# Optimization experiments

Hardware: AMD Instinct MI355X
Metric: run time of the kernel (lower is better)

Reference implementation:

```python
import jax, jax.numpy as jnp
from jax import lax
import numpy as np

B, P, N = 4, 12000, 100   # batch, max_pillars, max_points_per_pillar
H, W = 108, 124           # pseudo-image size from forward()
DN = ('NCHW', 'HWIO', 'NCHW')


def _conv(x, k, b):
    y = lax.conv_general_dilated(x, k, (1, 1), 'SAME', dimension_numbers=DN)
    return y + b[None, :, None, None]


def _cbr(x, k, b, s, t):
    # Conv2d + folded BatchNorm2d (eval: per-channel scale/shift) + ReLU
    y = _conv(x, k, b)
    return jax.nn.relu(y * s[None, :, None, None] + t[None, :, None, None])


def _pool(x):
    return lax.reduce_window(x, -jnp.inf, lax.max, (1, 1, 2, 2), (1, 1, 2, 2), 'VALID')


def setup_inputs() -> dict:
    key = jax.random.key(0)
    ks = iter(jax.random.split(key, 64))
    d = {}
    d['pillars'] = jax.random.normal(next(ks), (B, P, N, 9), jnp.float32)

    def w(shape, scale=0.05):
        return jax.random.normal(next(ks), shape, jnp.float32) * scale

    d['w1'] = w((9, 64)); d['b1'] = w((64,))
    d['s1'] = 1.0 + w((64,)); d['t1'] = w((64,))
    d['w2'] = w((64, 64)); d['b2'] = w((64,))
    d['s2'] = 1.0 + w((64,)); d['t2'] = w((64,))
    chans = [(64, 64), (64, 64), (64, 128), (128, 128), (128, 256), (256, 256)]
    for i, (ci, co) in enumerate(chans, 1):
        d['ck%d' % i] = w((3, 3, ci, co)); d['cb%d' % i] = w((co,))
        d['cs%d' % i] = 1.0 + w((co,)); d['ct%d' % i] = w((co,))
    d['hk1'] = w((3, 3, 256, 256)); d['hb1'] = w((256,))
    d['hk2'] = w((1, 1, 256, 10)); d['hb2'] = w((10,))
    d['num_points'] = jax.random.randint(next(ks), (B, P), 0, 100, jnp.int32)
    return d


def reference(pillars, w1, b1, s1, t1, w2, b2, s2, t2,
              ck1, cb1, cs1, ct1, ck2, cb2, cs2, ct2,
              ck3, cb3, cs3, ct3, ck4, cb4, cs4, ct4,
              ck5, cb5, cs5, ct5, ck6, cb6, cs6, ct6,
              hk1, hb1, hk2, hb2, num_points):
    # pillar feature net: Linear+BN(folded)+ReLU x2, batched over all points  [B,P,N,9] -> [B,P,N,64]
    h = jax.nn.relu((pillars @ w1 + b1) * s1 + t1)
    h = jax.nn.relu((h @ w2 + b2) * s2 + t2)
    # masked segment-max over the variable-length point groups
    mask = jnp.arange(N)[None, None, :] < num_points[:, :, None]          # [B,P,N]
    neg = jnp.finfo(h.dtype).min
    feat = jnp.max(jnp.where(mask[..., None], h, neg), axis=2)            # [B,P,64]
    valid = num_points > 0
    feat = jnp.where(valid[..., None], feat, 0.0)
    cnt = jnp.maximum(jnp.sum(valid, axis=1), 1).astype(feat.dtype)       # [B]
    mean = jnp.sum(feat, axis=1) / cnt[:, None]                           # [B,64]
    # nearest-interpolate a 1x1 map to HxW == broadcast
    x = jnp.broadcast_to(mean[:, :, None, None], (pillars.shape[0], 64, H, W))
    # 2D backbone
    x = _cbr(x, ck1, cb1, cs1, ct1); x = _cbr(x, ck2, cb2, cs2, ct2); x = _pool(x)
    x = _cbr(x, ck3, cb3, cs3, ct3); x = _cbr(x, ck4, cb4, cs4, ct4); x = _pool(x)
    x = _cbr(x, ck5, cb5, cs5, ct5); x = _cbr(x, ck6, cb6, cs6, ct6)
    # detection head
    y = jax.nn.relu(_conv(x, hk1, hb1))
    return _conv(y, hk2, hb2)   # [B, num_classes+7=10, 27, 31]
```

## Files before the change

kernel.cpp:

```cpp
#include <hip/hip_runtime.h>

typedef __bf16 vbf8 __attribute__((ext_vector_type(8)));
typedef unsigned short us8 __attribute__((ext_vector_type(8)));
typedef float f32x4 __attribute__((ext_vector_type(4)));
typedef float f32x4u __attribute__((ext_vector_type(4), aligned(4)));

#define NBLK 64

__device__ __forceinline__ int caseof(int h, int H, int e) {
  if (h < 0 || h >= H) return -1;
  if (h < e) return h;
  if (h >= H - e) return h - (H - 1) + 2 * e;
  return e;
}
__device__ __forceinline__ int repof(int i, int H, int eo) {
  return (i <= eo) ? i : H - 1 - 2 * eo + i;
}

__device__ __forceinline__ vbf8 max8(vbf8 a, vbf8 b) {
  us8 ua = __builtin_bit_cast(us8, a), ub = __builtin_bit_cast(us8, b);
  us8 o;
#pragma unroll
  for (int e = 0; e < 8; ++e) o[e] = ua[e] > ub[e] ? ua[e] : ub[e];
  return __builtin_bit_cast(vbf8, o);
}

__device__ __forceinline__ void gridbar(int* bar) {
  __syncthreads();
  if (threadIdx.x == 0) {
    int* cnt = bar; int* gen = bar + 1;
    int g = __hip_atomic_fetch_add(gen, 0, __ATOMIC_RELAXED, __HIP_MEMORY_SCOPE_AGENT);
    if (__hip_atomic_fetch_add(cnt, 1, __ATOMIC_ACQ_REL, __HIP_MEMORY_SCOPE_AGENT) == NBLK - 1) {
      __hip_atomic_fetch_add(cnt, -NBLK, __ATOMIC_RELAXED, __HIP_MEMORY_SCOPE_AGENT);
      __hip_atomic_fetch_add(gen, 1, __ATOMIC_RELEASE, __HIP_MEMORY_SCOPE_AGENT);
    } else {
      while (__hip_atomic_fetch_add(gen, 0, __ATOMIC_RELAXED, __HIP_MEMORY_SCOPE_AGENT) == g)
        __builtin_amdgcn_s_sleep(32);
    }
  }
  __syncthreads();
  __builtin_amdgcn_fence(__ATOMIC_ACQUIRE, "agent");
}

__global__ void setup_kernel(const float* __restrict__ w1, const float* __restrict__ b1,
                             const float* __restrict__ s1, const float* __restrict__ t1,
                             const float* __restrict__ w2, const float* __restrict__ b2,
                             const float* __restrict__ s2, const float* __restrict__ t2,
                             __bf16* __restrict__ wfrag, float* __restrict__ be2f) {
  int l = threadIdx.x;
  int s = l & 15, g = l >> 4;
#pragma unroll
  for (int m = 0; m < 4; ++m) {
    int c = 32 * (m & 1) + 8 * (s >> 2) + 4 * (m >> 1) + (s & 3);
#pragma unroll
    for (int e = 0; e < 8; ++e) {
      int k = g * 8 + e;
      float v = 0.f;
      if (k < 9)       v = w1[k * 64 + c] * s1[c];
      else if (k == 9) v = fmaf(b1[c], s1[c], t1[c]);
      wfrag[(m * 64 + l) * 8 + e] = (__bf16)v;
    }
    int co = s + 16 * m;
#pragma unroll
    for (int e = 0; e < 8; ++e) {
      int k = g * 8 + e;
      wfrag[((4 + m) * 64 + l) * 8 + e] = (__bf16)(w2[k * 64 + co] * s2[co]);
      wfrag[((8 + m) * 64 + l) * 8 + e] = (__bf16)(w2[(32 + k) * 64 + co] * s2[co]);
    }
    be2f[m * 64 + l] = fmaf(b2[co], s2[co], t2[co]);
  }
}

__global__ __launch_bounds__(256) void convw_kernel(
    const float* __restrict__ k1, const float* __restrict__ k2,
    const float* __restrict__ k3, const float* __restrict__ k4,
    const float* __restrict__ k5, const float* __restrict__ k6,
    const float* __restrict__ kh, __bf16* __restrict__ wT) {
  __shared__ float tile[64][65];
  const int tCI[7]    = {64, 64, 64, 128, 128, 256, 256};
  const int tCO[7]    = {64, 64, 128, 128, 256, 256, 256};
  const int tOFF[7]   = {0, 36864, 73728, 147456, 294912, 589824, 1179648};
  const int tTILES[7] = {9, 9, 18, 36, 72, 144, 144};
  int bid = blockIdx.x;
  int ti = 0, acc = 0;
  while (ti < 6 && bid >= acc + tTILES[ti]) { acc += tTILES[ti]; ++ti; }
  int lt = bid - acc;
  int CI = tCI[ti], CO = tCO[ti];
  const float* src;
  if (ti == 0) src = k1; else if (ti == 1) src = k2; else if (ti == 2) src = k3;
  else if (ti == 3) src = k4; else if (ti == 4) src = k5; else if (ti == 5) src = k6;
  else src = kh;
  int cot = CO / 64, tpt = (CI / 64) * cot;
  int tap = lt / tpt; int r2 = lt - tap * tpt;
  int ci0 = (r2 / cot) * 64, co0 = (r2 % cot) * 64;
  const float* sp = src + (size_t)(tap * CI + ci0) * CO + co0;
  int t = threadIdx.x;
  int lr = t >> 6, lc = t & 63;
#pragma unroll
  for (int rr = 0; rr < 64; rr += 4)
    tile[rr + lr][lc] = sp[(size_t)(rr + lr) * CO + lc];
  __syncthreads();
  __bf16* dst = wT + tOFF[ti] + ((size_t)tap * CO + co0) * CI + ci0;
#pragma unroll
  for (int rr = 0; rr < 64; rr += 4)
    dst[(size_t)(rr + lr) * CI + lc] = (__bf16)tile[lc][rr + lr];
}

__global__ __launch_bounds__(256) void pillar_kernel(
    const float* __restrict__ pil, const int* __restrict__ npt,
    const __bf16* __restrict__ wfrag, const float* __restrict__ be2f,
    float* __restrict__ partial, int* __restrict__ pcnt)
{
  __shared__ float redf[4][64];
  __shared__ int redc[4];
  const int tid = threadIdx.x;
  const int wv = tid >> 6, lane = tid & 63;
  const int s = lane & 15, g = lane >> 4;
  const int wid = blockIdx.x * 4 + wv;
  const int b = wid / 6000;
  const int p0 = (wid - b * 6000) * 2;

  vbf8 w1f[4], w2f0[4], w2f1[4];
  float be2[4];
#pragma unroll
  for (int m = 0; m < 4; ++m) {
    w1f[m]  = *(const vbf8*)(wfrag + ((0 + m) * 64 + lane) * 8);
    w2f0[m] = *(const vbf8*)(wfrag + ((4 + m) * 64 + lane) * 8);
    w2f1[m] = *(const vbf8*)(wfrag + ((8 + m) * 64 + lane) * 8);
    be2[m] = be2f[m * 64 + lane];
  }

  float fsum[4] = {0.f, 0.f, 0.f, 0.f};
  int cnt = 0;

  for (int i = 0; i < 2; ++i) {
    int pidx = b * 12000 + p0 + i;
    int np = npt[pidx];
    if (np <= 0) continue;
    ++cnt;
    float feat[4][4];
#pragma unroll
    for (int n = 0; n < 4; ++n)
#pragma unroll
      for (int r = 0; r < 4; ++r) feat[n][r] = 0.f;

    int ngrp = (np + 15) >> 4;
    const float* pbase = pil + (size_t)pidx * 900;
    const float* pp0 = pbase + s * 9;
    f32x4u lo = *(const f32x4u*)pp0;
    f32x4u hi = *(const f32x4u*)(pp0 + 4);
    float v8 = pp0[8];
    for (int grp = 0; grp < ngrp; ++grp) {
      int g2 = min(grp + 1, ngrp - 1);
      int ptn = min(g2 * 16 + s, 99);
      const float* ppn = pbase + ptn * 9;
      f32x4u nlo = *(const f32x4u*)ppn;
      f32x4u nhi = *(const f32x4u*)(ppn + 4);
      float nv8 = ppn[8];

      vbf8 b1f;
      b1f[0] = (__bf16)(g == 0 ? lo[0] : (g == 1 ? v8 : 0.f));
      b1f[1] = (__bf16)(g == 0 ? lo[1] : (g == 1 ? 1.0f : 0.f));
      b1f[2] = (__bf16)(g == 0 ? lo[2] : 0.f);
      b1f[3] = (__bf16)(g == 0 ? lo[3] : 0.f);
      b1f[4] = (__bf16)(g == 0 ? hi[0] : 0.f);
      b1f[5] = (__bf16)(g == 0 ? hi[1] : 0.f);
      b1f[6] = (__bf16)(g == 0 ? hi[2] : 0.f);
      b1f[7] = (__bf16)(g == 0 ? hi[3] : 0.f);

      const f32x4 z = {0.f, 0.f, 0.f, 0.f};
      f32x4 d1[4];
#pragma unroll
      for (int m = 0; m < 4; ++m)
        d1[m] = __builtin_amdgcn_mfma_f32_16x16x32_bf16(w1f[m], b1f, z, 0, 0, 0);

      vbf8 a2f0, a2f1;
#pragma unroll
      for (int r = 0; r < 4; ++r) {
        a2f0[r]     = (__bf16)fmaxf(d1[0][r], 0.f);
        a2f1[r]     = (__bf16)fmaxf(d1[1][r], 0.f);
        a2f0[4 + r] = (__bf16)fmaxf(d1[2][r], 0.f);
        a2f1[4 + r] = (__bf16)fmaxf(d1[3][r], 0.f);
      }

      f32x4 d2[4];
#pragma unroll
      for (int n = 0; n < 4; ++n) {
        f32x4 cb = {be2[n], be2[n], be2[n], be2[n]};
        d2[n] = __builtin_amdgcn_mfma_f32_16x16x32_bf16(a2f0, w2f0[n], cb, 0, 0, 0);
        d2[n] = __builtin_amdgcn_mfma_f32_16x16x32_bf16(a2f1, w2f1[n], d2[n], 0, 0, 0);
      }
      if (((grp + 1) << 4) <= np) {
#pragma unroll
        for (int n = 0; n < 4; ++n)
#pragma unroll
          for (int r = 0; r < 4; ++r) feat[n][r] = fmaxf(feat[n][r], d2[n][r]);
      } else {
#pragma unroll
        for (int n = 0; n < 4; ++n)
#pragma unroll
          for (int r = 0; r < 4; ++r) {
            float vv = (grp * 16 + 4 * g + r < np) ? d2[n][r] : 0.f;
            feat[n][r] = fmaxf(feat[n][r], vv);
          }
      }
      lo = nlo; hi = nhi; v8 = nv8;
    }
#pragma unroll
    for (int n = 0; n < 4; ++n) {
      float m = fmaxf(fmaxf(feat[n][0], feat[n][1]), fmaxf(feat[n][2], feat[n][3]));
      m = fmaxf(m, __shfl_xor(m, 16));
      m = fmaxf(m, __shfl_xor(m, 32));
      fsum[n] += m;
    }
  }
  if (g == 0) {
#pragma unroll
    for (int n = 0; n < 4; ++n) redf[wv][s + 16 * n] = fsum[n];
  }
  if (lane == 0) redc[wv] = cnt;
  __syncthreads();
  if (tid < 64) {
    float tot = redf[0][tid] + redf[1][tid] + redf[2][tid] + redf[3][tid];
    partial[blockIdx.x * 64 + tid] = tot;
    if (tid == 0) pcnt[blockIdx.x] = redc[0] + redc[1] + redc[2] + redc[3];
  }
}

__global__ void mean_kernel(const float* __restrict__ partial,
                            const int* __restrict__ pcnt,
                            __bf16* __restrict__ x0,
                            __bf16* __restrict__ zbuf, int* __restrict__ bar) {
  int b = blockIdx.x, t = threadIdx.x;
  if (b == 0) {
    zbuf[t] = (__bf16)0.f;
    if (t < 2) bar[t] = 0;
  }
  int c = t & 63, q = t >> 6;
  float sum = 0.f;
  for (int w = q; w < 1500; w += 4) sum += partial[(b * 1500 + w) * 64 + c];
  int cl = 0;
  for (int w = t; w < 1500; w += 256) cl += pcnt[b * 1500 + w];
  __shared__ float sh[256];
  __shared__ int shc[256];
  sh[t] = sum; shc[t] = cl;
  __syncthreads();
  for (int o = 128; o > 0; o >>= 1) {
    if (t < o) shc[t] += shc[t + o];
    __syncthreads();
  }
  if (t < 64) {
    float tot = sh[t] + sh[t + 64] + sh[t + 128] + sh[t + 192];
    x0[b * 64 + t] = (__bf16)(tot / (float)(shc[0] > 0 ? shc[0] : 1));
  }
}

template <int CI, int CO, int H, int EIN, bool POOL, bool HAS_BN, bool OUT_F32>
__device__ __forceinline__ void caseconv_dev(
    int wid, const __bf16* __restrict__ xin, const __bf16* __restrict__ wt,
    const float* __restrict__ cb, const float* __restrict__ cs,
    const float* __restrict__ ct, __bf16* __restrict__ yout,
    float* __restrict__ yf32, const __bf16* __restrict__ zbuf)
{
  constexpr int EV   = POOL ? (EIN + 1) / 2 : EIN;
  constexpr int EOUT = EV + 1;
  constexpr int NBI  = 2 * EIN + 1;
  constexpr int HX   = POOL ? 2 * H : H;
  constexpr int NBO  = 2 * EOUT + 1;
  constexpr int M    = NBO * NBO * 4;
  constexpr int NT   = CO / 16;
  constexpr int KC   = CI / 32;
  constexpr int MT   = (M + 31) / 32;
  if (wid >= MT * NT) return;
  const int lane = threadIdx.x & 63;
  const int s = lane & 15, g = lane >> 4;
  const int nt = wid % NT, mt = wid / NT;

  int reph[2], repw[2], bsel[2];
#pragma unroll
  for (int mf = 0; mf < 2; ++mf) {
    int m = mt * 32 + mf * 16 + s; if (m >= M) m = M - 1;
    bsel[mf] = m & 3; int q = m >> 2;
    int bw = q % NBO, bh = q / NBO;
    reph[mf] = repof(bh, H, EOUT); repw[mf] = repof(bw, H, EOUT);
  }

  f32x4 acc0 = {0.f, 0.f, 0.f, 0.f}, acc1 = {0.f, 0.f, 0.f, 0.f};
#pragma unroll
  for (int tap = 0; tap < 9; ++tap) {
    const int dh = tap / 3, dw = tap % 3;
    const __bf16* wtap = wt + ((size_t)tap * CO + nt * 16) * CI + 8 * g;
    const __bf16* base[2][POOL ? 4 : 1];
#pragma unroll
    for (int mf = 0; mf < 2; ++mf) {
      int vh = reph[mf] + dh - 1, vw = repw[mf] + dw - 1;
      if constexpr (POOL) {
        bool valid = (vh >= 0) && (vh < H) && (vw >= 0) && (vw < H);
        int h0 = 0, h1 = 0, w0 = 0, w1 = 0;
        if (valid) {
          h0 = caseof(2 * vh, HX, EIN); h1 = caseof(2 * vh + 1, HX, EIN);
          w0 = caseof(2 * vw, HX, EIN); w1 = caseof(2 * vw + 1, HX, EIN);
        }
        base[mf][0] = valid ? xin + (size_t)((h0 * NBI + w0) * 4 + bsel[mf]) * CI : zbuf;
        base[mf][1] = valid ? xin + (size_t)((h0 * NBI + w1) * 4 + bsel[mf]) * CI : zbuf;
        base[mf][2] = valid ? xin + (size_t)((h1 * NBI + w0) * 4 + bsel[mf]) * CI : zbuf;
        base[mf][3] = valid ? xin + (size_t)((h1 * NBI + w1) * 4 + bsel[mf]) * CI : zbuf;
      } else {
        int jh = caseof(vh, H, EIN), jw = caseof(vw, H, EIN);
        bool v = (jh >= 0) && (jw >= 0);
        base[mf][0] = v ? xin + (size_t)((jh * NBI + jw) * 4 + bsel[mf]) * CI : zbuf;
      }
    }
#pragma unroll
    for (int ck = 0; ck < KC; ++ck) {
      vbf8 a0, a1;
      if constexpr (POOL) {
        a0 = max8(max8(*(const vbf8*)(base[0][0] + ck * 32 + 8 * g),
                       *(const vbf8*)(base[0][1] + ck * 32 + 8 * g)),
                  max8(*(const vbf8*)(base[0][2] + ck * 32 + 8 * g),
                       *(const vbf8*)(base[0][3] + ck * 32 + 8 * g)));
        a1 = max8(max8(*(const vbf8*)(base[1][0] + ck * 32 + 8 * g),
                       *(const vbf8*)(base[1][1] + ck * 32 + 8 * g)),
                  max8(*(const vbf8*)(base[1][2] + ck * 32 + 8 * g),
                       *(const vbf8*)(base[1][3] + ck * 32 + 8 * g)));
      } else {
        a0 = *(const vbf8*)(base[0][0] + ck * 32 + 8 * g);
        a1 = *(const vbf8*)(base[1][0] + ck * 32 + 8 * g);
      }
      vbf8 bb = *(const vbf8*)(wtap + (size_t)s * CI + ck * 32);
      acc0 = __builtin_amdgcn_mfma_f32_16x16x32_bf16(a0, bb, acc0, 0, 0, 0);
      acc1 = __builtin_amdgcn_mfma_f32_16x16x32_bf16(a1, bb, acc1, 0, 0, 0);
    }
  }

  int co = nt * 16 + s;
  float sc, sh;
  if (HAS_BN) { sc = cs[co]; sh = fmaf(cb[co], sc, ct[co]); }
  else        { sc = 1.f;    sh = cb[co]; }
#pragma unroll
  for (int mf = 0; mf < 2; ++mf) {
    f32x4 acc = mf ? acc1 : acc0;
#pragma unroll
    for (int r = 0; r < 4; ++r) {
      int m = mt * 32 + mf * 16 + 4 * g + r;
      if (m < M) {
        float v = fmaxf(fmaf(acc[r], sc, sh), 0.f);
        if constexpr (OUT_F32) yf32[(size_t)m * CO + co] = v;
        else                   yout[(size_t)m * CO + co] = (__bf16)v;
      }
    }
  }
}

__device__ __forceinline__ void headscatter_dev(int gtid, const float* __restrict__ x,
                                                const float* __restrict__ wk,
                                                const float* __restrict__ bias,
                                                float* __restrict__ out) {
  for (int idx = gtid; idx < 4 * 10 * 27 * 31; idx += NBLK * 256) {
    int c = idx % 31;
    int r = (idx / 31) % 27;
    int ch = (idx / (31 * 27)) % 10;
    int b = idx / (31 * 27 * 10);
    int rr = (r <= 7) ? r : ((r >= 20) ? r - 11 : 7);
    int cc = (c <= 7) ? c : ((c >= 24) ? c - 15 : 7);
    int ph = caseof(rr, 16, 5), pw = caseof(cc, 16, 5);
    const float* xr = x + (size_t)((ph * 11 + pw) * 4 + b) * 256;
    float a0 = 0.f, a1 = 0.f, a2 = 0.f, a3 = 0.f;
#pragma unroll 4
    for (int ci = 0; ci < 256; ci += 4) {
      float4 in4 = *(const float4*)(xr + ci);
      a0 = fmaf(in4.x, wk[(ci + 0) * 10 + ch], a0);
      a1 = fmaf(in4.y, wk[(ci + 1) * 10 + ch], a1);
      a2 = fmaf(in4.z, wk[(ci + 2) * 10 + ch], a2);
      a3 = fmaf(in4.w, wk[(ci + 3) * 10 + ch], a3);
    }
    out[idx] = (a0 + a1) + (a2 + a3) + bias[ch];
  }
}

__global__ __launch_bounds__(256) void backbone_kernel(
    const __bf16* __restrict__ X0, __bf16* __restrict__ X1, __bf16* __restrict__ X2,
    __bf16* __restrict__ X3, __bf16* __restrict__ X4, __bf16* __restrict__ X5,
    __bf16* __restrict__ X6, float* __restrict__ XH,
    const __bf16* wt1, const __bf16* wt2, const __bf16* wt3, const __bf16* wt4,
    const __bf16* wt5, const __bf16* wt6, const __bf16* wth,
    const float* cb1, const float* cs1, const float* ct1,
    const float* cb2, const float* cs2, const float* ct2,
    const float* cb3, const float* cs3, const float* ct3,
    const float* cb4, const float* cs4, const float* ct4,
    const float* cb5, const float* cs5, const float* ct5,
    const float* cb6, const float* cs6, const float* ct6,
    const float* hb1, const float* hk2, const float* hb2,
    const __bf16* __restrict__ zbuf, int* __restrict__ bar, float* __restrict__ out)
{
  const int wid = blockIdx.x * 4 + (threadIdx.x >> 6);
  const int gtid = blockIdx.x * 256 + threadIdx.x;

  caseconv_dev<64, 64, 64, 0, false, true, false>(wid, X0, wt1, cb1, cs1, ct1, X1, nullptr, zbuf);
  gridbar(bar);
  caseconv_dev<64, 64, 64, 1, false, true, false>(wid, X1, wt2, cb2, cs2, ct2, X2, nullptr, zbuf);
  gridbar(bar);
  caseconv_dev<64, 128, 32, 2, true, true, false>(wid, X2, wt3, cb3, cs3, ct3, X3, nullptr, zbuf);
  gridbar(bar);
  caseconv_dev<128, 128, 32, 2, false, true, false>(wid, X3, wt4, cb4, cs4, ct4, X4, nullptr, zbuf);
  gridbar(bar);
  caseconv_dev<128, 256, 16, 3, true, true, false>(wid, X4, wt5, cb5, cs5, ct5, X5, nullptr, zbuf);
  gridbar(bar);
  caseconv_dev<256, 256, 16, 3, false, true, false>(wid, X5, wt6, cb6, cs6, ct6, X6, nullptr, zbuf);
  gridbar(bar);
  caseconv_dev<256, 256, 16, 4, false, false, true>(wid, X6, wth, hb1, nullptr, nullptr, nullptr, XH, zbuf);
  gridbar(bar);
  headscatter_dev(gtid, XH, hk2, hb2, out);
}

extern "C" void kernel_launch(void* const* d_in, const int* in_sizes, int n_in,
                              void* d_out, int out_size, void* d_ws, size_t ws_size,
                              hipStream_t stream) {
  (void)in_sizes; (void)n_in; (void)out_size; (void)ws_size;
  const float* pillars = (const float*)d_in[0];
  const float* w1 = (const float*)d_in[1];
  const float* b1 = (const float*)d_in[2];
  const float* s1 = (const float*)d_in[3];
  const float* t1 = (const float*)d_in[4];
  const float* w2 = (const float*)d_in[5];
  const float* b2 = (const float*)d_in[6];
  const float* s2 = (const float*)d_in[7];
  const float* t2 = (const float*)d_in[8];
  const float* ck[6], *cbv[6], *csv[6], *ctv[6];
  for (int i = 0; i < 6; ++i) {
    ck[i]  = (const float*)d_in[9 + i * 4];
    cbv[i] = (const float*)d_in[10 + i * 4];
    csv[i] = (const float*)d_in[11 + i * 4];
    ctv[i] = (const float*)d_in[12 + i * 4];
  }
  const float* hk1 = (const float*)d_in[33];
  const float* hb1 = (const float*)d_in[34];
  const float* hk2 = (const float*)d_in[35];
  const float* hb2 = (const float*)d_in[36];
  const int* num_points = (const int*)d_in[37];
  float* out = (float*)d_out;

  char* wsb = (char*)d_ws;
  size_t off = 0;
  auto alloc = [&](size_t n) { char* p = wsb + off; off = (off + n + 255) & ~(size_t)255; return p; };
  float*  ppart = (float*)alloc(1536000);
  int*    pcnt  = (int*)alloc(24000);
  __bf16* wfrag = (__bf16*)alloc(12288);
  float*  be2f  = (float*)alloc(1024);
  __bf16* wT    = (__bf16*)alloc(3538944);
  __bf16* zbuf  = (__bf16*)alloc(512);
  int*    bar   = (int*)alloc(256);
  __bf16* X0    = (__bf16*)alloc(512);
  __bf16* X1    = (__bf16*)alloc(4608);
  __bf16* X2    = (__bf16*)alloc(12800);
  __bf16* X3    = (__bf16*)alloc(25600);
  __bf16* X4    = (__bf16*)alloc(50176);
  __bf16* X5    = (__bf16*)alloc(100352);
  __bf16* X6    = (__bf16*)alloc(165888);
  float*  XH    = (float*)alloc(495616);

  __bf16* wt1 = wT + 0;       __bf16* wt2 = wT + 36864;
  __bf16* wt3 = wT + 73728;   __bf16* wt4 = wT + 147456;
  __bf16* wt5 = wT + 294912;  __bf16* wt6 = wT + 589824;
  __bf16* wth = wT + 1179648;

  setup_kernel<<<1, 64, 0, stream>>>(w1, b1, s1, t1, w2, b2, s2, t2, wfrag, be2f);
  convw_kernel<<<432, 256, 0, stream>>>(ck[0], ck[1], ck[2], ck[3], ck[4], ck[5],
                                        hk1, wT);
  pillar_kernel<<<6000, 256, 0, stream>>>(pillars, num_points, wfrag, be2f,
                                          ppart, pcnt);
  mean_kernel<<<4, 256, 0, stream>>>(ppart, pcnt, X0, zbuf, bar);
  backbone_kernel<<<NBLK, 256, 0, stream>>>(
      X0, X1, X2, X3, X4, X5, X6, XH,
      wt1, wt2, wt3, wt4, wt5, wt6, wth,
      cbv[0], csv[0], ctv[0], cbv[1], csv[1], ctv[1],
      cbv[2], csv[2], ctv[2], cbv[3], csv[3], ctv[3],
      cbv[4], csv[4], ctv[4], cbv[5], csv[5], ctv[5],
      hb1, hk2, hb2, zbuf, bar, out);
}
```

Baseline: 390.5 us.

## Merge setup kernels, fuse mean and conv1-conv2 into backbone via LDS

Folds setup_kernel into the weight-transpose kernel as an extra block, removes mean_kernel by computing the per-batch mean inside the persistent backbone kernel, and fuses conv1 and conv2 per batch through shared memory to drop a grid barrier. It also halves the persistent grid to 32 blocks with a strided work loop and reworks the grid barrier to use plain loads/stores with shorter sleeps. This targets launch overhead and barrier latency in a latency-bound tail. The cost is less parallelism for the larger convs, and with fewer blocks each wave loops over more tiles.

```diff
diff --git a/kernel.cpp b/kernel.cpp
--- a/kernel.cpp
+++ b/kernel.cpp
@@ -5,7 +5,7 @@
 typedef float f32x4 __attribute__((ext_vector_type(4)));
 typedef float f32x4u __attribute__((ext_vector_type(4), aligned(4)));
 
-#define NBLK 64
+#define NBLK 32
 
 __device__ __forceinline__ int caseof(int h, int H, int e) {
   if (h < 0 || h >= H) return -1;
@@ -29,54 +29,64 @@
   __syncthreads();
   if (threadIdx.x == 0) {
     int* cnt = bar; int* gen = bar + 1;
-    int g = __hip_atomic_fetch_add(gen, 0, __ATOMIC_RELAXED, __HIP_MEMORY_SCOPE_AGENT);
+    int g = __hip_atomic_load(gen, __ATOMIC_RELAXED, __HIP_MEMORY_SCOPE_SYSTEM);
     if (__hip_atomic_fetch_add(cnt, 1, __ATOMIC_ACQ_REL, __HIP_MEMORY_SCOPE_AGENT) == NBLK - 1) {
-      __hip_atomic_fetch_add(cnt, -NBLK, __ATOMIC_RELAXED, __HIP_MEMORY_SCOPE_AGENT);
-      __hip_atomic_fetch_add(gen, 1, __ATOMIC_RELEASE, __HIP_MEMORY_SCOPE_AGENT);
+      __hip_atomic_store(cnt, 0, __ATOMIC_RELAXED, __HIP_MEMORY_SCOPE_AGENT);
+      __hip_atomic_store(gen, g + 1, __ATOMIC_RELEASE, __HIP_MEMORY_SCOPE_SYSTEM);
     } else {
-      while (__hip_atomic_fetch_add(gen, 0, __ATOMIC_RELAXED, __HIP_MEMORY_SCOPE_AGENT) == g)
-        __builtin_amdgcn_s_sleep(32);
+      while (__hip_atomic_load(gen, __ATOMIC_RELAXED, __HIP_MEMORY_SCOPE_SYSTEM) == g)
+        __builtin_amdgcn_s_sleep(4);
+      __builtin_amdgcn_fence(__ATOMIC_ACQUIRE, "agent");
     }
   }
   __syncthreads();
-  __builtin_amdgcn_fence(__ATOMIC_ACQUIRE, "agent");
-}
-
-__global__ void setup_kernel(const float* __restrict__ w1, const float* __restrict__ b1,
-                             const float* __restrict__ s1, const float* __restrict__ t1,
-                             const float* __restrict__ w2, const float* __restrict__ b2,
-                             const float* __restrict__ s2, const float* __restrict__ t2,
-                             __bf16* __restrict__ wfrag, float* __restrict__ be2f) {
-  int l = threadIdx.x;
-  int s = l & 15, g = l >> 4;
-#pragma unroll
-  for (int m = 0; m < 4; ++m) {
-    int c = 32 * (m & 1) + 8 * (s >> 2) + 4 * (m >> 1) + (s & 3);
-#pragma unroll
-    for (int e = 0; e < 8; ++e) {
-      int k = g * 8 + e;
-      float v = 0.f;
-      if (k < 9)       v = w1[k * 64 + c] * s1[c];
-      else if (k == 9) v = fmaf(b1[c], s1[c], t1[c]);
-      wfrag[(m * 64 + l) * 8 + e] = (__bf16)v;
-    }
-    int co = s + 16 * m;
-#pragma unroll
-    for (int e = 0; e < 8; ++e) {
-      int k = g * 8 + e;
-      wfrag[((4 + m) * 64 + l) * 8 + e] = (__bf16)(w2[k * 64 + co] * s2[co]);
-      wfrag[((8 + m) * 64 + l) * 8 + e] = (__bf16)(w2[(32 + k) * 64 + co] * s2[co]);
-    }
-    be2f[m * 64 + l] = fmaf(b2[co], s2[co], t2[co]);
-  }
-}
-
-__global__ __launch_bounds__(256) void convw_kernel(
+}
+
+__global__ __launch_bounds__(256) void prep_kernel(
     const float* __restrict__ k1, const float* __restrict__ k2,
     const float* __restrict__ k3, const float* __restrict__ k4,
     const float* __restrict__ k5, const float* __restrict__ k6,
-    const float* __restrict__ kh, __bf16* __restrict__ wT) {
+    const float* __restrict__ kh, __bf16* __restrict__ wT,
+    const float* __restrict__ w1, const float* __restrict__ b1,
+    const float* __restrict__ s1, const float* __restrict__ t1,
+    const float* __restrict__ w2, const float* __restrict__ b2,
+    const float* __restrict__ s2, const float* __restrict__ t2,
+    __bf16* __restrict__ wfrag, float* __restrict__ be2f,
+    __bf16* __restrict__ zbuf, int* __restrict__ bar) {
   __shared__ float tile[64][65];
+  if (blockIdx.x == 432) {
+    int l = threadIdx.x;
+    if (l < 64) {
+      int s = l & 15, g = l >> 4;
+#pragma unroll
+      for (int m = 0; m < 4; ++m) {
+        int c = 32 * (m & 1) + 8 * (s >> 2) + 4 * (m >> 1) + (s & 3);
+#pragma unroll
+        for (int e = 0; e < 8; ++e) {
+          int k = g * 8 + e;
+          float v = 0.f;
+          if (k < 9)       v = w1[k * 64 + c] * s1[c];
+          else if (k == 9) v = fmaf(b1[c], s1[c], t1[c]);
+          wfrag[(m * 64 + l) * 8 + e] = (__bf16)v;
+        }
+        int co = s + 16 * m;
+#pragma unroll
+        for (int e = 0; e < 8; ++e) {
+          int k = g * 8 + e;
+          wfrag[((4 + m) * 64 + l) * 8 + e] = (__bf16)(w2[k * 64 + co] * s2[co]);
+          wfrag[((8 + m) * 64 + l) * 8 + e] = (__bf16)(w2[(32 + k) * 64 + co] * s2[co]);
+        }
+        be2f[m * 64 + l] = fmaf(b2[co], s2[co], t2[co]);
+      }
+    } else if (l >= 64 && l < 128) {
+      int z = l - 64;
+#pragma unroll
+      for (int i = 0; i < 4; ++i) zbuf[z * 4 + i] = (__bf16)0.f;
+    } else if (l == 128) {
+      bar[0] = 0; bar[1] = 0;
+    }
+    return;
+  }
   const int tCI[7]    = {64, 64, 64, 128, 128, 256, 256};
   const int tCO[7]    = {64, 64, 128, 128, 256, 256, 256};
   const int tOFF[7]   = {0, 36864, 73728, 147456, 294912, 589824, 1179648};
@@ -227,37 +237,9 @@
   }
 }
 
-__global__ void mean_kernel(const float* __restrict__ partial,
-                            const int* __restrict__ pcnt,
-                            __bf16* __restrict__ x0,
-                            __bf16* __restrict__ zbuf, int* __restrict__ bar) {
-  int b = blockIdx.x, t = threadIdx.x;
-  if (b == 0) {
-    zbuf[t] = (__bf16)0.f;
-    if (t < 2) bar[t] = 0;
-  }
-  int c = t & 63, q = t >> 6;
-  float sum = 0.f;
-  for (int w = q; w < 1500; w += 4) sum += partial[(b * 1500 + w) * 64 + c];
-  int cl = 0;
-  for (int w = t; w < 1500; w += 256) cl += pcnt[b * 1500 + w];
-  __shared__ float sh[256];
-  __shared__ int shc[256];
-  sh[t] = sum; shc[t] = cl;
-  __syncthreads();
-  for (int o = 128; o > 0; o >>= 1) {
-    if (t < o) shc[t] += shc[t + o];
-    __syncthreads();
-  }
-  if (t < 64) {
-    float tot = sh[t] + sh[t + 64] + sh[t + 128] + sh[t + 192];
-    x0[b * 64 + t] = (__bf16)(tot / (float)(shc[0] > 0 ? shc[0] : 1));
-  }
-}
-
 template <int CI, int CO, int H, int EIN, bool POOL, bool HAS_BN, bool OUT_F32>
 __device__ __forceinline__ void caseconv_dev(
-    int wid, const __bf16* __restrict__ xin, const __bf16* __restrict__ wt,
+    int wid0, const __bf16* __restrict__ xin, const __bf16* __restrict__ wt,
     const float* __restrict__ cb, const float* __restrict__ cs,
     const float* __restrict__ ct, __bf16* __restrict__ yout,
     float* __restrict__ yf32, const __bf16* __restrict__ zbuf)
@@ -271,117 +253,93 @@
   constexpr int NT   = CO / 16;
   constexpr int KC   = CI / 32;
   constexpr int MT   = (M + 31) / 32;
-  if (wid >= MT * NT) return;
   const int lane = threadIdx.x & 63;
   const int s = lane & 15, g = lane >> 4;
-  const int nt = wid % NT, mt = wid / NT;
-
-  int reph[2], repw[2], bsel[2];
-#pragma unroll
-  for (int mf = 0; mf < 2; ++mf) {
-    int m = mt * 32 + mf * 16 + s; if (m >= M) m = M - 1;
-    bsel[mf] = m & 3; int q = m >> 2;
-    int bw = q % NBO, bh = q / NBO;
-    reph[mf] = repof(bh, H, EOUT); repw[mf] = repof(bw, H, EOUT);
-  }
-
-  f32x4 acc0 = {0.f, 0.f, 0.f, 0.f}, acc1 = {0.f, 0.f, 0.f, 0.f};
-#pragma unroll
-  for (int tap = 0; tap < 9; ++tap) {
-    const int dh = tap / 3, dw = tap % 3;
-    const __bf16* wtap = wt + ((size_t)tap * CO + nt * 16) * CI + 8 * g;
-    const __bf16* base[2][POOL ? 4 : 1];
+
+  for (int wid = wid0; wid < MT * NT; wid += NBLK * 4) {
+    const int nt = wid % NT, mt = wid / NT;
+    int reph[2], repw[2], bsel[2];
 #pragma unroll
     for (int mf = 0; mf < 2; ++mf) {
-      int vh = reph[mf] + dh - 1, vw = repw[mf] + dw - 1;
-      if constexpr (POOL) {
-        bool valid = (vh >= 0) && (vh < H) && (vw >= 0) && (vw < H);
-        int h0 = 0, h1 = 0, w0 = 0, w1 = 0;
-        if (valid) {
-          h0 = caseof(2 * vh, HX, EIN); h1 = caseof(2 * vh + 1, HX, EIN);
-          w0 = caseof(2 * vw, HX, EIN); w1 = caseof(2 * vw + 1, HX, EIN);
-        }
-        base[mf][0] = valid ? xin + (size_t)((h0 * NBI + w0) * 4 + bsel[mf]) * CI : zbuf;
-        base[mf][1] = valid ? xin + (size_t)((h0 * NBI + w1) * 4 + bsel[mf]) * CI : zbuf;
-        base[mf][2] = valid ? xin + (size_t)((h1 * NBI + w0) * 4 + bsel[mf]) * CI : zbuf;
-        base[mf][3] = valid ? xin + (size_t)((h1 * NBI + w1) * 4 + bsel[mf]) * CI : zbuf;
-      } else {
-        int jh = caseof(vh, H, EIN), jw = caseof(vw, H, EIN);
-        bool v = (jh >= 0) && (jw >= 0);
-        base[mf][0] = v ? xin + (size_t)((jh * NBI + jw) * 4 + bsel[mf]) * CI : zbuf;
-      }
-    }
-#pragma unroll
-    for (int ck = 0; ck < KC; ++ck) {
-      vbf8 a0, a1;
-      if constexpr (POOL) {
-        a0 = max8(max8(*(const vbf8*)(base[0][0] + ck * 32 + 8 * g),
-                       *(const vbf8*)(base[0][1] + ck * 32 + 8 * g)),
-                  max8(*(const vbf8*)(base[0][2] + ck * 32 + 8 * g),
-                       *(const vbf8*)(base[0][3] + ck * 32 + 8 * g)));
-        a1 = max8(max8(*(const vbf8*)(base[1][0] + ck * 32 + 8 * g),
-                       *(const vbf8*)(base[1][1] + ck * 32 + 8 * g)),
-                  max8(*(const vbf8*)(base[1][2] + ck * 32 + 8 * g),
-                       *(const vbf8*)(base[1][3] + ck * 32 + 8 * g)));
-      } else {
-        a0 = *(const vbf8*)(base[0][0] + ck * 32 + 8 * g);
-        a1 = *(const vbf8*)(base[1][0] + ck * 32 + 8 * g);
-      }
-      vbf8 bb = *(const vbf8*)(wtap + (size_t)s * CI + ck * 32);
-      acc0 = __builtin_amdgcn_mfma_f32_16x16x32_bf16(a0, bb, acc0, 0, 0, 0);
-      acc1 = __builtin_amdgcn_mfma_f32_16x16x32_bf16(a1, bb, acc1, 0, 0, 0);
-    }
-  }
-
-  int co = nt * 16 + s;
-  float sc, sh;
-  if (HAS_BN) { sc = cs[co]; sh = fmaf(cb[co], sc, ct[co]); }
-  else        { sc = 1.f;    sh = cb[co]; }
-#pragma unroll
-  for (int mf = 0; mf < 2; ++mf) {
-    f32x4 acc = mf ? acc1 : acc0;
-#pragma unroll
-    for (int r = 0; r < 4; ++r) {
-      int m = mt * 32 + mf * 16 + 4 * g + r;
-      if (m < M) {
-        float v = fmaxf(fmaf(acc[r], sc, sh), 0.f);
-        if constexpr (OUT_F32) yf32[(size_t)m * CO + co] = v;
-        else                   yout[(size_t)m * CO + co] = (__bf16)v;
-      }
-    }
-  }
-}
-
-__device__ __forceinline__ void headscatter_dev(int gtid, const float* __restrict__ x,
-                                                const float* __restrict__ wk,
-                                                const float* __restrict__ bias,
-                                                float* __restrict__ out) {
-  for (int idx = gtid; idx < 4 * 10 * 27 * 31; idx += NBLK * 256) {
-    int c = idx % 31;
-    int r = (idx / 31) % 27;
-    int ch = (idx / (31 * 27)) % 10;
-    int b = idx / (31 * 27 * 10);
-    int rr = (r <= 7) ? r : ((r >= 20) ? r - 11 : 7);
-    int cc = (c <= 7) ? c : ((c >= 24) ? c - 15 : 7);
-    int ph = caseof(rr, 16, 5), pw = caseof(cc, 16, 5);
-    const float* xr = x + (size_t)((ph * 11 + pw) * 4 + b) * 256;
-    float a0 = 0.f, a1 = 0.f, a2 = 0.f, a3 = 0.f;
-#pragma unroll 4
-    for (int ci = 0; ci < 256; ci += 4) {
-      float4 in4 = *(const float4*)(xr + ci);
-      a0 = fmaf(in4.x, wk[(ci + 0) * 10 + ch], a0);
-      a1 = fmaf(in4.y, wk[(ci + 1) * 10 + ch], a1);
-      a2 = fmaf(in4.z, wk[(ci + 2) * 10 + ch], a2);
-      a3 = fmaf(in4.w, wk[(ci + 3) * 10 + ch], a3);
-    }
-    out[idx] = (a0 + a1) + (a2 + a3) + bias[ch];
+      int m = mt * 32 + mf * 16 + s; if (m >= M) m = M - 1;
+      bsel[mf] = m & 3; int q = m >> 2;
+      int bw = q % NBO, bh = q / NBO;
+      reph[mf] = repof(bh, H, EOUT); repw[mf] = repof(bw, H, EOUT);
+    }
+
+    f32x4 acc0 = {0.f, 0.f, 0.f, 0.f}, acc1 = {0.f, 0.f, 0.f, 0.f};
+#pragma unroll
+    for (int tap = 0; tap < 9; ++tap) {
+      const int dh = tap / 3, dw = tap % 3;
+      const __bf16* wtap = wt + ((size_t)tap * CO + nt * 16) * CI + 8 * g;
+      const __bf16* base[2][POOL ? 4 : 1];
+#pragma unroll
+      for (int mf = 0; mf < 2; ++mf) {
+        int vh = reph[mf] + dh - 1, vw = repw[mf] + dw - 1;
+        if constexpr (POOL) {
+          bool valid = (vh >= 0) && (vh < H) && (vw >= 0) && (vw < H);
+          int h0 = 0, h1 = 0, w0 = 0, w1 = 0;
+          if (valid) {
+            h0 = caseof(2 * vh, HX, EIN); h1 = caseof(2 * vh + 1, HX, EIN);
+            w0 = caseof(2 * vw, HX, EIN); w1 = caseof(2 * vw + 1, HX, EIN);
+          }
+          base[mf][0] = valid ? xin + (size_t)((h0 * NBI + w0) * 4 + bsel[mf]) * CI : zbuf;
+          base[mf][1] = valid ? xin + (size_t)((h0 * NBI + w1) * 4 + bsel[mf]) * CI : zbuf;
+          base[mf][2] = valid ? xin + (size_t)((h1 * NBI + w0) * 4 + bsel[mf]) * CI : zbuf;
+          base[mf][3] = valid ? xin + (size_t)((h1 * NBI + w1) * 4 + bsel[mf]) * CI : zbuf;
+        } else {
+          int jh = caseof(vh, H, EIN), jw = caseof(vw, H, EIN);
+          bool v = (jh >= 0) && (jw >= 0);
+          base[mf][0] = v ? xin + (size_t)((jh * NBI + jw) * 4 + bsel[mf]) * CI : zbuf;
+        }
+      }
+#pragma unroll
+      for (int ck = 0; ck < KC; ++ck) {
+        vbf8 a0, a1;
+        if constexpr (POOL) {
+          a0 = max8(max8(*(const vbf8*)(base[0][0] + ck * 32 + 8 * g),
+                         *(const vbf8*)(base[0][1] + ck * 32 + 8 * g)),
+                    max8(*(const vbf8*)(base[0][2] + ck * 32 + 8 * g),
+                         *(const vbf8*)(base[0][3] + ck * 32 + 8 * g)));
+          a1 = max8(max8(*(const vbf8*)(base[1][0] + ck * 32 + 8 * g),
+                         *(const vbf8*)(base[1][1] + ck * 32 + 8 * g)),
+                    max8(*(const vbf8*)(base[1][2] + ck * 32 + 8 * g),
+                         *(const vbf8*)(base[1][3] + ck * 32 + 8 * g)));
+        } else {
+          a0 = *(const vbf8*)(base[0][0] + ck * 32 + 8 * g);
+          a1 = *(const vbf8*)(base[1][0] + ck * 32 + 8 * g);
+        }
+        vbf8 bb = *(const vbf8*)(wtap + (size_t)s * CI + ck * 32);
+        acc0 = __builtin_amdgcn_mfma_f32_16x16x32_bf16(a0, bb, acc0, 0, 0, 0);
+        acc1 = __builtin_amdgcn_mfma_f32_16x16x32_bf16(a1, bb, acc1, 0, 0, 0);
+      }
+    }
+
+    int co = nt * 16 + s;
+    float sc, sh;
+    if (HAS_BN) { sc = cs[co]; sh = fmaf(cb[co], sc, ct[co]); }
+    else        { sc = 1.f;    sh = cb[co]; }
+#pragma unroll
+    for (int mf = 0; mf < 2; ++mf) {
+      f32x4 acc = mf ? acc1 : acc0;
+#pragma unroll
+      for (int r = 0; r < 4; ++r) {
+        int m = mt * 32 + mf * 16 + 4 * g + r;
+        if (m < M) {
+          float v = fmaxf(fmaf(acc[r], sc, sh), 0.f);
+          if constexpr (OUT_F32) yf32[(size_t)m * CO + co] = v;
+          else                   yout[(size_t)m * CO + co] = (__bf16)v;
+        }
+      }
+    }
   }
 }
 
 __global__ __launch_bounds__(256) void backbone_kernel(
-    const __bf16* __restrict__ X0, __bf16* __restrict__ X1, __bf16* __restrict__ X2,
-    __bf16* __restrict__ X3, __bf16* __restrict__ X4, __bf16* __restrict__ X5,
-    __bf16* __restrict__ X6, float* __restrict__ XH,
+    const float* __restrict__ ppart, const int* __restrict__ pcnt,
+    __bf16* __restrict__ X0, __bf16* __restrict__ X2, __bf16* __restrict__ X3,
+    __bf16* __restrict__ X4, __bf16* __restrict__ X5, __bf16* __restrict__ X6,
+    float* __restrict__ XH,
     const __bf16* wt1, const __bf16* wt2, const __bf16* wt3, const __bf16* wt4,
     const __bf16* wt5, const __bf16* wt6, const __bf16* wth,
     const float* cb1, const float* cs1, const float* ct1,
@@ -391,14 +349,133 @@
     const float* cb5, const float* cs5, const float* ct5,
     const float* cb6, const float* cs6, const float* ct6,
     const float* hb1, const float* hk2, const float* hb2,
-    const __bf16* __restrict__ zbuf, int* __restrict__ bar, float* __restrict__ out)
+    const __bf16* __restrict__ zbuf, int* __restrict__ bar,
+    float* __restrict__ out)
 {
-  const int wid = blockIdx.x * 4 + (threadIdx.x >> 6);
-  const int gtid = blockIdx.x * 256 + threadIdx.x;
-
-  caseconv_dev<64, 64, 64, 0, false, true, false>(wid, X0, wt1, cb1, cs1, ct1, X1, nullptr, zbuf);
-  gridbar(bar);
-  caseconv_dev<64, 64, 64, 1, false, true, false>(wid, X1, wt2, cb2, cs2, ct2, X2, nullptr, zbuf);
+  __shared__ __bf16 ldsX1[36 * 64];
+  __shared__ __bf16 zp[64];
+  const int tid = threadIdx.x;
+  const int wv = tid >> 6, lane = tid & 63;
+  const int s = lane & 15, g = lane >> 4;
+  const int wid = blockIdx.x * 4 + wv;
+  const int gtid = blockIdx.x * 256 + tid;
+
+  if (blockIdx.x < 4) {
+    int b = blockIdx.x;
+    int c = tid & 63, q = tid >> 6;
+    float sum = 0.f;
+    for (int w = q; w < 1500; w += 4) sum += ppart[(b * 1500 + w) * 64 + c];
+    int cl = 0;
+    for (int w = tid; w < 1500; w += 256) cl += pcnt[b * 1500 + w];
+    __shared__ float sh[256];
+    __shared__ int shc[256];
+    sh[tid] = sum; shc[tid] = cl;
+    __syncthreads();
+    for (int o = 128; o > 0; o >>= 1) {
+      if (tid < o) shc[tid] += shc[tid + o];
+      __syncthreads();
+    }
+    if (tid < 64) {
+      float tot = sh[tid] + sh[tid + 64] + sh[tid + 128] + sh[tid + 192];
+      X0[b * 64 + tid] = (__bf16)(tot / (float)(shc[0] > 0 ? shc[0] : 1));
+    }
+  }
+  if (tid < 64) zp[tid] = (__bf16)0.f;
+  gridbar(bar);
+
+  if (blockIdx.x < 4) {
+    for (int t8 = wv; t8 < 8; t8 += 4) {
+      int nt = t8 & 3, mt = t8 >> 2;
+      int reph[2], repw[2], bsel[2];
+#pragma unroll
+      for (int mf = 0; mf < 2; ++mf) {
+        int m = mt * 32 + mf * 16 + s; if (m >= 36) m = 35;
+        bsel[mf] = m & 3; int q = m >> 2;
+        int bw = q % 3, bh = q / 3;
+        reph[mf] = repof(bh, 64, 1); repw[mf] = repof(bw, 64, 1);
+      }
+      f32x4 acc0 = {0.f, 0.f, 0.f, 0.f}, acc1 = {0.f, 0.f, 0.f, 0.f};
+#pragma unroll
+      for (int tap = 0; tap < 9; ++tap) {
+        int dh = tap / 3, dw = tap % 3;
+        const __bf16* wtap = wt1 + ((size_t)tap * 64 + nt * 16) * 64 + 8 * g;
+        const __bf16* pa[2];
+#pragma unroll
+        for (int mf = 0; mf < 2; ++mf) {
+          int vh = reph[mf] + dh - 1, vw = repw[mf] + dw - 1;
+          bool v = (vh >= 0) && (vh < 64) && (vw >= 0) && (vw < 64);
+          pa[mf] = v ? X0 + bsel[mf] * 64 : zbuf;
+        }
+#pragma unroll
+        for (int ck = 0; ck < 2; ++ck) {
+          vbf8 a0 = *(const vbf8*)(pa[0] + ck * 32 + 8 * g);
+          vbf8 a1 = *(const vbf8*)(pa[1] + ck * 32 + 8 * g);
+          vbf8 bb = *(const vbf8*)(wtap + (size_t)s * 64 + ck * 32);
+          acc0 = __builtin_amdgcn_mfma_f32_16x16x32_bf16(a0, bb, acc0, 0, 0, 0);
+          acc1 = __builtin_amdgcn_mfma_f32_16x16x32_bf16(a1, bb, acc1, 0, 0, 0);
+        }
+      }
+      int co = nt * 16 + s;
+      float sc = cs1[co], shv = fmaf(cb1[co], sc, ct1[co]);
+#pragma unroll
+      for (int mf = 0; mf < 2; ++mf) {
+        f32x4 acc = mf ? acc1 : acc0;
+#pragma unroll
+        for (int r = 0; r < 4; ++r) {
+          int m = mt * 32 + mf * 16 + 4 * g + r;
+          if (m < 36)
+            ldsX1[m * 64 + co] = (__bf16)fmaxf(fmaf(acc[r], sc, shv), 0.f);
+        }
+      }
+    }
+    __syncthreads();
+    {
+      int t16 = blockIdx.x * 4 + wv;
+      int nt = t16 & 3, mt = t16 >> 2;
+      int reph[2], repw[2], bsel[2];
+#pragma unroll
+      for (int mf = 0; mf < 2; ++mf) {
+        int m = mt * 32 + mf * 16 + s; if (m >= 100) m = 99;
+        bsel[mf] = m & 3; int q = m >> 2;
+        int bw = q % 5, bh = q / 5;
+        reph[mf] = repof(bh, 64, 2); repw[mf] = repof(bw, 64, 2);
+      }
+      f32x4 acc0 = {0.f, 0.f, 0.f, 0.f}, acc1 = {0.f, 0.f, 0.f, 0.f};
+#pragma unroll
+      for (int tap = 0; tap < 9; ++tap) {
+        int dh = tap / 3, dw = tap % 3;
+        const __bf16* wtap = wt2 + ((size_t)tap * 64 + nt * 16) * 64 + 8 * g;
+        const __bf16* pa[2];
+#pragma unroll
+        for (int mf = 0; mf < 2; ++mf) {
+          int jh = caseof(reph[mf] + dh - 1, 64, 1);
+          int jw = caseof(repw[mf] + dw - 1, 64, 1);
+          bool v = (jh >= 0) && (jw >= 0);
+          pa[mf] = v ? ldsX1 + ((jh * 3 + jw) * 4 + bsel[mf]) * 64 : zp;
+        }
+#pragma unroll
+        for (int ck = 0; ck < 2; ++ck) {
+          vbf8 a0 = *(const vbf8*)(pa[0] + ck * 32 + 8 * g);
+          vbf8 a1 = *(const vbf8*)(pa[1] + ck * 32 + 8 * g);
+          vbf8 bb = *(const vbf8*)(wtap + (size_t)s * 64 + ck * 32);
+          acc0 = __builtin_amdgcn_mfma_f32_16x16x32_bf16(a0, bb, acc0, 0, 0, 0);
+          acc1 = __builtin_amdgcn_mfma_f32_16x16x32_bf16(a1, bb, acc1, 0, 0, 0);
+        }
+      }
+      int co = nt * 16 + s;
+      float sc = cs2[co], shv = fmaf(cb2[co], sc, ct2[co]);
+#pragma unroll
+      for (int mf = 0; mf < 2; ++mf) {
+        f32x4 acc = mf ? acc1 : acc0;
+#pragma unroll
+        for (int r = 0; r < 4; ++r) {
+          int m = mt * 32 + mf * 16 + 4 * g + r;
+          if (m < 100)
+            X2[(size_t)m * 64 + co] = (__bf16)fmaxf(fmaf(acc[r], sc, shv), 0.f);
+        }
+      }
+    }
+  }
   gridbar(bar);
   caseconv_dev<64, 128, 32, 2, true, true, false>(wid, X2, wt3, cb3, cs3, ct3, X3, nullptr, zbuf);
   gridbar(bar);
@@ -410,7 +487,26 @@
   gridbar(bar);
   caseconv_dev<256, 256, 16, 4, false, false, true>(wid, X6, wth, hb1, nullptr, nullptr, nullptr, XH, zbuf);
   gridbar(bar);
-  headscatter_dev(gtid, XH, hk2, hb2, out);
+  for (int idx = gtid; idx < 4 * 10 * 27 * 31; idx += NBLK * 256) {
+    int c = idx % 31;
+    int r = (idx / 31) % 27;
+    int ch = (idx / (31 * 27)) % 10;
+    int b = idx / (31 * 27 * 10);
+    int rr = (r <= 7) ? r : ((r >= 20) ? r - 11 : 7);
+    int cc = (c <= 7) ? c : ((c >= 24) ? c - 15 : 7);
+    int ph = caseof(rr, 16, 5), pw = caseof(cc, 16, 5);
+    const float* xr = XH + (size_t)((ph * 11 + pw) * 4 + b) * 256;
+    float a0 = 0.f, a1 = 0.f, a2 = 0.f, a3 = 0.f;
+#pragma unroll 4
+    for (int ci = 0; ci < 256; ci += 4) {
+      float4 in4 = *(const float4*)(xr + ci);
+      a0 = fmaf(in4.x, hk2[(ci + 0) * 10 + ch], a0);
+      a1 = fmaf(in4.y, hk2[(ci + 1) * 10 + ch], a1);
+      a2 = fmaf(in4.z, hk2[(ci + 2) * 10 + ch], a2);
+      a3 = fmaf(in4.w, hk2[(ci + 3) * 10 + ch], a3);
+    }
+    out[idx] = (a0 + a1) + (a2 + a3) + hb2[ch];
+  }
 }
 
 extern "C" void kernel_launch(void* const* d_in, const int* in_sizes, int n_in,
@@ -451,7 +547,6 @@
   __bf16* zbuf  = (__bf16*)alloc(512);
   int*    bar   = (int*)alloc(256);
   __bf16* X0    = (__bf16*)alloc(512);
-  __bf16* X1    = (__bf16*)alloc(4608);
   __bf16* X2    = (__bf16*)alloc(12800);
   __bf16* X3    = (__bf16*)alloc(25600);
   __bf16* X4    = (__bf16*)alloc(50176);
@@ -464,14 +559,13 @@
   __bf16* wt5 = wT + 294912;  __bf16* wt6 = wT + 589824;
   __bf16* wth = wT + 1179648;
 
-  setup_kernel<<<1, 64, 0, stream>>>(w1, b1, s1, t1, w2, b2, s2, t2, wfrag, be2f);
-  convw_kernel<<<432, 256, 0, stream>>>(ck[0], ck[1], ck[2], ck[3], ck[4], ck[5],
-                                        hk1, wT);
+  prep_kernel<<<433, 256, 0, stream>>>(ck[0], ck[1], ck[2], ck[3], ck[4], ck[5],
+                                       hk1, wT, w1, b1, s1, t1, w2, b2, s2, t2,
+                                       wfrag, be2f, zbuf, bar);
   pillar_kernel<<<6000, 256, 0, stream>>>(pillars, num_points, wfrag, be2f,
                                           ppart, pcnt);
-  mean_kernel<<<4, 256, 0, stream>>>(ppart, pcnt, X0, zbuf, bar);
   backbone_kernel<<<NBLK, 256, 0, stream>>>(
-      X0, X1, X2, X3, X4, X5, X6, XH,
+      ppart, pcnt, X0, X2, X3, X4, X5, X6, XH,
       wt1, wt2, wt3, wt4, wt5, wt6, wth,
       cbv[0], csv[0], ctv[0], cbv[1], csv[1], ctv[1],
       cbv[2], csv[2], ctv[2], cbv[3], csv[3], ctv[3],
```

Measured after the change: 414.4 us. +6.1%, slower.
